# Kernel tuning notes

Measured on AMD Instinct MI355X. Metric: run time of the kernel, lower is better.

## Reference

```python
import jax, jax.numpy as jnp
import numpy as np

N = 50000      # nodes
E = 1600000    # edges (avg degree 32)
DIM = 128
HEADS = 8
HEAD_DIM = DIM // HEADS
HID = 4 * DIM          # hidden_multiplier=4 -> 512
FF_IN = 2 * DIM        # input_multiplier=2 (concat [h, message])
SCALE = 0.02


def setup_inputs() -> dict:
    key = jax.random.key(0)
    ks = jax.random.split(key, 13)
    h = jax.random.normal(ks[0], (N, DIM), dtype=jnp.float32)
    src = jax.random.randint(ks[1], (E,), 0, N, dtype=jnp.int32)
    dst = jax.random.randint(ks[2], (E,), 0, N, dtype=jnp.int32)
    W_in = jax.random.normal(ks[3], (DIM, DIM), dtype=jnp.float32) * SCALE
    b_in = jnp.zeros((DIM,), dtype=jnp.float32)
    Wu = jax.random.normal(ks[4], (DIM, HEADS), dtype=jnp.float32) * SCALE
    bu = jnp.zeros((HEADS,), dtype=jnp.float32)
    Wv = jax.random.normal(ks[5], (DIM, HEADS), dtype=jnp.float32) * SCALE  # no bias
    W1 = jax.random.normal(ks[6], (FF_IN, HID), dtype=jnp.float32) * SCALE
    b1 = jnp.zeros((HID,), dtype=jnp.float32)
    W2 = jax.random.normal(ks[7], (HID, DIM), dtype=jnp.float32) * SCALE
    b2 = jnp.zeros((DIM,), dtype=jnp.float32)
    return dict(h=h, W_in=W_in, b_in=b_in, Wu=Wu, bu=bu, Wv=Wv,
                W1=W1, b1=b1, W2=W2, b2=b2, src=src, dst=dst)


def reference(h, W_in, b_in, Wu, bu, Wv, W1, b1, W2, b2, src, dst):
    # input projection
    h1 = h @ W_in + b_in                                  # [N, DIM]
    attn_u = h1 @ Wu + bu                                 # [N, H]
    attn_v = h1 @ Wv                                      # [N, H]
    # u_add_v + LeakyReLU(0.2): per-edge scores
    scores = attn_u[src] + attn_v[dst]                    # [E, H]
    scores = jnp.where(scores >= 0, scores, 0.2 * scores)
    # edge_softmax: normalize over edges incoming to each dst node
    smax = jax.ops.segment_max(scores, dst, num_segments=N)  # [N, H]
    smax = jnp.where(jnp.isfinite(smax), smax, jnp.zeros_like(smax))
    e = jnp.exp(scores - smax[dst])                       # [E, H]
    denom = jax.ops.segment_sum(e, dst, num_segments=N)   # [N, H]
    probs = e / denom[dst]                                # [E, H]
    # u_mul_e_sum with h reshaped to [N, head_dim, heads]
    h_heads = h1.reshape(N, HEAD_DIM, HEADS)
    msg = jax.ops.segment_sum(h_heads[src] * probs[:, None, :], dst,
                              num_segments=N).reshape(N, DIM)
    # feed-forward on concat (dropout = identity in eval)
    combined = jnp.concatenate([h1, msg], axis=1)         # [N, 2*DIM]
    x = jax.nn.gelu(combined @ W1 + b1, approximate=False)
    return x @ W2 + b2                                    # [N, DIM]
```

## Files before the change

kernel.cpp:

```cpp
#include <hip/hip_runtime.h>
#include <hip/hip_fp16.h>
#include <math.h>

#define DIMM 128
#define NHEAD 8
#define SLOTS 96
#define QCAP32 4352
#define NSLICE 128
#define RS 6272
#define NPAD 50176

typedef __attribute__((ext_vector_type(8))) short bf16x8;
typedef __attribute__((ext_vector_type(4))) float f32x4;
typedef __attribute__((ext_vector_type(2))) float f32x2;
typedef __attribute__((ext_vector_type(4))) int i32x4;

#if defined(__has_builtin)
#if __has_builtin(__builtin_amdgcn_cvt_pk_f32_fp8)
#define HAS_CVT_FP8 1
#endif
#endif

__device__ __forceinline__ unsigned short f2bf(float x) {
    union { float f; unsigned int u; } v; v.f = x;
    unsigned int r = v.u + 0x7FFFu + ((v.u >> 16) & 1u);
    return (unsigned short)(r >> 16);
}
__device__ __forceinline__ float bf2f(unsigned short u) {
    union { unsigned int u; float f; } v; v.u = ((unsigned int)u) << 16;
    return v.f;
}
__device__ __forceinline__ unsigned char f2e4m3(float x) {
    union { float f; unsigned u; } v; v.f = x;
    unsigned s = (v.u >> 24) & 0x80u;
    unsigned au = v.u & 0x7fffffffu;
    unsigned r = au + 0xFFFFFu + ((au >> 20) & 1u);
    int E = (int)(r >> 23) - 120;
    if (E < 1) return (unsigned char)s;
    if (E > 15) E = 15;
    return (unsigned char)(s | (E << 3) | ((r >> 20) & 7u));
}
__device__ __forceinline__ float e4m32f(unsigned b) {
    unsigned em = b & 0x7fu;
    unsigned s = (b & 0x80u) << 24;
    unsigned u = s | ((em + 960u) << 20);
    union { unsigned u; float f; } v;
    v.u = em ? u : s;
    return v.f;
}
__device__ __forceinline__ float gelu_exact(float x) {
    return 0.5f * x * (1.0f + erff(x * 0.70710678118654752f));
}
__device__ __forceinline__ __half2 shfl_xor_h2(__half2 v, int d) {
    union { __half2 h; int i; } u; u.h = v;
    u.i = __shfl_xor(u.i, d, 64);
    return u.h;
}

__global__ __launch_bounds__(256) void k_prep0(
        const float* __restrict__ W_in,
        unsigned short* __restrict__ WiT_hi, unsigned short* __restrict__ WiT_lo)
{
    int i = blockIdx.x * 256 + threadIdx.x;
    if (i < 128 * 128) {
        int n = i >> 7, k = i & 127;
        float w = W_in[(size_t)k * 128 + n];
        unsigned short hi = f2bf(w);
        WiT_hi[i] = hi;
        WiT_lo[i] = f2bf(w - bf2f(hi));
    }
}

__global__ __launch_bounds__(256, 4) void k_front(
        const float* __restrict__ h,
        const unsigned short* __restrict__ WiT_hi,
        const unsigned short* __restrict__ WiT_lo,
        const float* __restrict__ b_in,
        const float* __restrict__ Wu, const float* __restrict__ bu,
        const float* __restrict__ Wv,
        const float* __restrict__ W1, const float* __restrict__ W2,
        const int* __restrict__ src, const int* __restrict__ dst,
        unsigned short* __restrict__ h1c,
        unsigned short* __restrict__ hg8,
        unsigned short* __restrict__ au, unsigned short* __restrict__ av,
        unsigned short* __restrict__ W1T, unsigned short* __restrict__ W2T,
        unsigned short* __restrict__ gh,
        unsigned int* __restrict__ gq,
        int* __restrict__ gqn,
        int N, int E, int NH1, int SC)
{
    __shared__ unsigned long long smem64[QCAP32 / 2];
    __shared__ unsigned int hist32[RS / 2];
    __shared__ int qn;
    int b = blockIdx.x;
    int t = threadIdx.x;

    if (b < SC) {
        unsigned int* q32 = (unsigned int*)smem64;
        int range = b & 7;
        int slice = b >> 3;
        for (int i = t; i < RS / 2; i += 256) hist32[i] = 0;
        if (t == 0) qn = 0;
        __syncthreads();
        int per = (((E + NSLICE - 1) / NSLICE) + 3) & ~3;
        int s0 = slice * per;
        int s1 = min(s0 + per, E);
        int base_d = range * RS;
        int lane = t & 63;
        for (int be = s0; be < s1; be += 1024) {
            int e0 = be + t * 4;
            int dv[4] = {-1, -1, -1, -1};
            if (e0 + 3 < s1) {
                i32x4 d4 = __builtin_nontemporal_load((const i32x4*)(dst + e0));
                dv[0] = d4.x; dv[1] = d4.y; dv[2] = d4.z; dv[3] = d4.w;
            } else if (e0 < s1) {
                dv[0] = dst[e0];
                if (e0 + 1 < s1) dv[1] = dst[e0 + 1];
                if (e0 + 2 < s1) dv[2] = dst[e0 + 2];
            }
            int dl[4];
            bool m[4];
            int mcnt = 0;
            #pragma unroll
            for (int k = 0; k < 4; ++k) {
                dl[k] = dv[k] - base_d;
                m[k] = (unsigned)dl[k] < (unsigned)RS;
                mcnt += m[k] ? 1 : 0;
            }
            int incl = mcnt;
            #pragma unroll
            for (int d = 1; d < 64; d <<= 1) {
                int v = __shfl_up(incl, d, 64);
                if (lane >= d) incl += v;
            }
            int wb = 0;
            if (lane == 63 && incl) wb = atomicAdd(&qn, incl);
            wb = __shfl(wb, 63, 64);
            int pos = wb + incl - mcnt;
            #pragma unroll
            for (int k = 0; k < 4; ++k) {
                if (m[k]) {
                    int s = __builtin_nontemporal_load(src + e0 + k);
                    atomicAdd(&hist32[dl[k] >> 1], 1u << ((dl[k] & 1) * 16));
                    if (pos < QCAP32)
                        q32[pos] = ((unsigned)dl[k] << 16) | ((unsigned)s & 0xffffu);
                    ++pos;
                }
            }
        }
        __syncthreads();
        int M = min(qn, QCAP32);
        for (int i = t; i < M; i += 256)
            gq[(size_t)b * QCAP32 + i] = q32[i];
        if (t == 0) gqn[b] = M;
        unsigned int* ghrow = (unsigned int*)(gh + (size_t)slice * NPAD + base_d);
        for (int i = t; i < RS / 2; i += 256) ghrow[i] = hist32[i];
        return;
    }
    if (b >= SC + NH1) {
        int i = (b - SC - NH1) * 256 + t;
        if (i < 256 * 512) {
            int k = i >> 9, j = i & 511;
            W1T[(size_t)j * 256 + k] = f2bf(W1[i]);
        }
        if (i < 512 * 128) {
            int k = i >> 7, j = i & 127;
            W2T[(size_t)j * 512 + k] = f2bf(W2[i]);
        }
        return;
    }

    unsigned short* Ahi = (unsigned short*)smem64;
    unsigned short* Alo = Ahi + 32 * 136;
    float* Wuv = (float*)hist32;
    int row0 = (b - SC) * 32;
    int lane = t & 63, wv = t >> 6;
    const int g = lane >> 4, r16 = lane & 15;

    for (int i = t; i < 2048; i += 256) {
        int k = i >> 4, hh = i & 15;
        Wuv[i] = (hh < 8) ? Wu[k * 8 + hh] : Wv[k * 8 + (hh - 8)];
    }

    #pragma unroll
    for (int u = 0; u < 4; ++u) {
        int idx = t + u * 256;
        int r = idx >> 5, c4 = idx & 31;
        float4 v = make_float4(0.f, 0.f, 0.f, 0.f);
        if (row0 + r < N) v = *(const float4*)(h + (size_t)(row0 + r) * DIMM + c4 * 4);
        unsigned short hi[4], lo[4];
        float vv[4] = {v.x, v.y, v.z, v.w};
        #pragma unroll
        for (int q = 0; q < 4; ++q) {
            hi[q] = f2bf(vv[q]);
            lo[q] = f2bf(vv[q] - bf2f(hi[q]));
        }
        unsigned int h01 = (unsigned)hi[0] | ((unsigned)hi[1] << 16);
        unsigned int h23 = (unsigned)hi[2] | ((unsigned)hi[3] << 16);
        unsigned int l01 = (unsigned)lo[0] | ((unsigned)lo[1] << 16);
        unsigned int l23 = (unsigned)lo[2] | ((unsigned)lo[3] << 16);
        *(uint2*)&Ahi[r * 136 + c4 * 4] = make_uint2(h01, h23);
        *(uint2*)&Alo[r * 136 + c4 * 4] = make_uint2(l01, l23);
    }
    __syncthreads();

    f32x4 acc[2][2];
    #pragma unroll
    for (int mf = 0; mf < 2; ++mf)
        #pragma unroll
        for (int nf = 0; nf < 2; ++nf)
            acc[mf][nf] = (f32x4){0.f, 0.f, 0.f, 0.f};

    for (int ks = 0; ks < 128; ks += 32) {
        bf16x8 ahi[2], alo[2], bhi[2], blo[2];
        #pragma unroll
        for (int mf = 0; mf < 2; ++mf) {
            ahi[mf] = *(const bf16x8*)&Ahi[(mf * 16 + r16) * 136 + ks + g * 8];
            alo[mf] = *(const bf16x8*)&Alo[(mf * 16 + r16) * 136 + ks + g * 8];
        }
        #pragma unroll
        for (int nf = 0; nf < 2; ++nf) {
            int coln = wv * 32 + nf * 16 + r16;
            bhi[nf] = *(const bf16x8*)(WiT_hi + (size_t)coln * 128 + ks + g * 8);
            blo[nf] = *(const bf16x8*)(WiT_lo + (size_t)coln * 128 + ks + g * 8);
        }
        #pragma unroll
        for (int mf = 0; mf < 2; ++mf)
            #pragma unroll
            for (int nf = 0; nf < 2; ++nf) {
                acc[mf][nf] = __builtin_amdgcn_mfma_f32_16x16x32_bf16(
                                  ahi[mf], bhi[nf], acc[mf][nf], 0, 0, 0);
                acc[mf][nf] = __builtin_amdgcn_mfma_f32_16x16x32_bf16(
                                  ahi[mf], blo[nf], acc[mf][nf], 0, 0, 0);
                acc[mf][nf] = __builtin_amdgcn_mfma_f32_16x16x32_bf16(
                                  alo[mf], bhi[nf], acc[mf][nf], 0, 0, 0);
            }
    }
    __syncthreads();

    #pragma unroll
    for (int nf = 0; nf < 2; ++nf) {
        int col = wv * 32 + nf * 16 + r16;
        float bb = b_in[col];
        #pragma unroll
        for (int mf = 0; mf < 2; ++mf) {
            #pragma unroll
            for (int q = 0; q < 4; ++q) {
                int row = mf * 16 + g * 4 + q;
                unsigned short hb = f2bf(acc[mf][nf][q] + bb);
                Ahi[row * 136 + col] = hb;
                if (row0 + row < N) h1c[(size_t)(row0 + row) * 128 + col] = hb;
            }
        }
    }
    __syncthreads();

    {
        int r = t >> 3;
        int j = t & 7;
        int hh2 = (j & 3) * 2;
        bool isv = (j >= 4);
        int hb = (isv ? 8 : 0) + hh2;
        float a0 = isv ? 0.f : bu[hh2];
        float a1 = isv ? 0.f : bu[hh2 + 1];
        for (int k = 0; k < 128; k += 8) {
            bf16x8 h8 = *(const bf16x8*)&Ahi[r * 136 + k];
            #pragma unroll
            for (int q = 0; q < 8; ++q) {
                float hv = bf2f((unsigned short)h8[q]);
                a0 = fmaf(hv, Wuv[(k + q) * 16 + hb], a0);
                a1 = fmaf(hv, Wuv[(k + q) * 16 + hb + 1], a1);
            }
        }
        if (row0 + r < N) {
            unsigned int pk = (unsigned)f2bf(a0) | ((unsigned)f2bf(a1) << 16);
            if (!isv) *(unsigned int*)(au + (size_t)(row0 + r) * 8 + hh2) = pk;
            else      *(unsigned int*)(av + (size_t)(row0 + r) * 8 + hh2) = pk;
        }
    }

    {
        int l = t & 63;
        int rg = t >> 6;
        #pragma unroll
        for (int rr = 0; rr < 8; ++rr) {
            int r2 = rg * 8 + rr;
            if (row0 + r2 < N) {
                unsigned lo8 = f2e4m3(bf2f(Ahi[r2 * 136 + l]));
                unsigned hi8 = f2e4m3(bf2f(Ahi[r2 * 136 + l + 64]));
                hg8[(size_t)(row0 + r2) * 64 + l] = (unsigned short)((hi8 << 8) | lo8);
            }
        }
    }
}

__global__ __launch_bounds__(256) void k_scan2(
        const unsigned short* __restrict__ gh,
        unsigned short* __restrict__ gb,
        int* __restrict__ cnt)
{
    int d = blockIdx.x * 256 + threadIdx.x;
    int sum = 0;
    #pragma unroll 8
    for (int s = 0; s < NSLICE; ++s) {
        gb[(size_t)s * NPAD + d] = (unsigned short)sum;
        sum += gh[(size_t)s * NPAD + d];
    }
    cnt[d] = sum;
}

__global__ __launch_bounds__(256) void k_place(
        const unsigned int* __restrict__ gq,
        const int* __restrict__ gqn,
        const unsigned short* __restrict__ gb,
        unsigned short* __restrict__ slots)
{
    __shared__ int bases[RS];
    int b = blockIdx.x;
    int range = b & 7, slice = b >> 3;
    int t = threadIdx.x;
    const unsigned short* gbrow = gb + (size_t)slice * NPAD + range * RS;
    for (int i = t; i < RS; i += 256) bases[i] = (int)gbrow[i];
    __syncthreads();
    int M = gqn[b];
    const unsigned int* q = gq + (size_t)b * QCAP32;
    for (int i = t; i < M; i += 256) {
        unsigned u = q[i];
        int dl = (int)(u >> 16);
        int slot = atomicAdd(&bases[dl], 1);
        if (slot < SLOTS)
            slots[(size_t)(range * RS + dl) * SLOTS + slot] = (unsigned short)(u & 0xffffu);
    }
}

__global__ __launch_bounds__(256) void k_agg(
        const unsigned short* __restrict__ hg8,
        const unsigned short* __restrict__ au,
        const unsigned short* __restrict__ av,
        const int* __restrict__ cnt, const unsigned short* __restrict__ slots,
        unsigned short* __restrict__ msgc,
        int N)
{
    __shared__ float p_lds[4][8][68];
    __shared__ int   s_lds[4][64];
    int t = threadIdx.x;
    int w = t >> 6, lane = t & 63;
    int n = blockIdx.x * 4 + w;
    if (n >= N) return;
    int deg = min(cnt[n], SLOTS);
    const unsigned short* myslots = slots + (size_t)n * SLOTS;
    unsigned short* msg_out = msgc + (size_t)n * 128;
    if (deg == 0) {
        msg_out[lane] = 0;
        msg_out[64 + lane] = 0;
        return;
    }

    float avf[8];
    {
        bf16x8 a8 = *(const bf16x8*)(av + (size_t)n * 8);
        #pragma unroll
        for (int hh = 0; hh < 8; ++hh) avf[hh] = bf2f((unsigned short)a8[hh]);
    }
    int hsel = lane & 7;
    float den = 0.f, accA = 0.f, accB = 0.f;

    for (int base = 0; base < deg; base += 64) {
        int nact = min(64, deg - base);
        bool act = (lane < nact);
        int sn = act ? (int)myslots[base + lane] : 0;
        float p[8];
        if (act) {
            bf16x8 u8 = *(const bf16x8*)(au + (size_t)sn * 8);
            #pragma unroll
            for (int hh = 0; hh < 8; ++hh) {
                float v = bf2f((unsigned short)u8[hh]) + avf[hh];
                v = (v >= 0.f) ? v : 0.2f * v;
                p[hh] = __expf(v);
            }
        } else {
            #pragma unroll
            for (int hh = 0; hh < 8; ++hh) p[hh] = 0.f;
        }

        __half2 PS[4];
        #pragma unroll
        for (int q = 0; q < 4; ++q) PS[q] = __floats2half2_rn(p[2*q], p[2*q+1]);
        #pragma unroll
        for (int d = 1; d < 8; d <<= 1) {
            #pragma unroll
            for (int q = 0; q < 4; ++q)
                PS[q] = __hadd2(PS[q], shfl_xor_h2(PS[q], d));
        }
        __half2 s01 = (hsel & 2) ? PS[1] : PS[0];
        __half2 s23 = (hsel & 2) ? PS[3] : PS[2];
        __half2 sel = (hsel & 4) ? s23 : s01;
        float csum_own = (hsel & 1) ? __high2float(sel) : __low2float(sel);
        #pragma unroll
        for (int d = 8; d < 64; d <<= 1)
            csum_own += __shfl_xor(csum_own, d, 64);
        den += csum_own;

        #pragma unroll
        for (int hh = 0; hh < 8; ++hh) p_lds[w][hh][lane] = p[hh];
        s_lds[w][lane] = sn;
        __threadfence_block();

        #pragma unroll 4
        for (int j = 0; j < nact; ++j) {
            int sj = s_lds[w][j];
            float pj = p_lds[w][hsel][j];
            unsigned int gg = (unsigned)hg8[(size_t)sj * 64 + lane];
#ifdef HAS_CVT_FP8
            f32x2 vv = __builtin_amdgcn_cvt_pk_f32_fp8((int)gg, false);
            accA = fmaf(pj, vv[0], accA);
            accB = fmaf(pj, vv[1], accB);
#else
            accA = fmaf(pj, e4m32f(gg & 0xffu), accA);
            accB = fmaf(pj, e4m32f(gg >> 8), accB);
#endif
        }
    }
    float inv = 1.0f / den;
    msg_out[lane] = f2bf(accA * inv);
    msg_out[64 + lane] = f2bf(accB * inv);
}

__global__ __launch_bounds__(256, 2) void k_ff(
        const unsigned short* __restrict__ h1c,
        const unsigned short* __restrict__ msgc,
        const unsigned short* __restrict__ W1T, const float* __restrict__ b1,
        const unsigned short* __restrict__ W2T, const float* __restrict__ b2,
        float* __restrict__ out, int N)
{
    __shared__ unsigned short smem[64 * 520];
    int t = threadIdx.x;
    int lane = t & 63, w = t >> 6;
    int row0 = blockIdx.x * 64;
    const int g = lane >> 4, r16 = lane & 15;

    #pragma unroll
    for (int u = 0; u < 8; ++u) {
        int idx = t + u * 256;
        int r = idx >> 5, c8 = idx & 31;
        bf16x8 v = {0, 0, 0, 0, 0, 0, 0, 0};
        if (row0 + r < N) {
            const unsigned short* sp = (c8 < 16)
                ? (h1c  + (size_t)(row0 + r) * 128 + c8 * 8)
                : (msgc + (size_t)(row0 + r) * 128 + (c8 - 16) * 8);
            v = *(const bf16x8*)sp;
        }
        *(bf16x8*)&smem[r * 264 + c8 * 8] = v;
    }
    __syncthreads();

    f32x4 acc[4][8];
    #pragma unroll
    for (int mf = 0; mf < 4; ++mf)
        #pragma unroll
        for (int nf = 0; nf < 8; ++nf)
            acc[mf][nf] = (f32x4){0.f, 0.f, 0.f, 0.f};

    int wcol = w * 128;
    for (int ks = 0; ks < 256; ks += 32) {
        bf16x8 a[4], b[8];
        #pragma unroll
        for (int mf = 0; mf < 4; ++mf)
            a[mf] = *(const bf16x8*)&smem[(mf * 16 + r16) * 264 + ks + g * 8];
        #pragma unroll
        for (int nf = 0; nf < 8; ++nf)
            b[nf] = *(const bf16x8*)(W1T + (size_t)(wcol + nf * 16 + r16) * 256 + ks + g * 8);
        #pragma unroll
        for (int mf = 0; mf < 4; ++mf)
            #pragma unroll
            for (int nf = 0; nf < 8; ++nf)
                acc[mf][nf] = __builtin_amdgcn_mfma_f32_16x16x32_bf16(
                                  a[mf], b[nf], acc[mf][nf], 0, 0, 0);
    }
    __syncthreads();

    #pragma unroll
    for (int nf = 0; nf < 8; ++nf) {
        int col = wcol + nf * 16 + r16;
        float bb = b1[col];
        #pragma unroll
        for (int mf = 0; mf < 4; ++mf) {
            #pragma unroll
            for (int q = 0; q < 4; ++q) {
                int row = mf * 16 + g * 4 + q;
                smem[row * 520 + col] = f2bf(gelu_exact(acc[mf][nf][q] + bb));
            }
        }
    }
    __syncthreads();

    f32x4 acc2[4][2];
    #pragma unroll
    for (int mf = 0; mf < 4; ++mf)
        #pragma unroll
        for (int nf = 0; nf < 2; ++nf)
            acc2[mf][nf] = (f32x4){0.f, 0.f, 0.f, 0.f};

    int ocol = w * 32;
    for (int ks = 0; ks < 512; ks += 32) {
        bf16x8 a[4], b[2];
        #pragma unroll
        for (int mf = 0; mf < 4; ++mf)
            a[mf] = *(const bf16x8*)&smem[(mf * 16 + r16) * 520 + ks + g * 8];
        #pragma unroll
        for (int nf = 0; nf < 2; ++nf)
            b[nf] = *(const bf16x8*)(W2T + (size_t)(ocol + nf * 16 + r16) * 512 + ks + g * 8);
        #pragma unroll
        for (int mf = 0; mf < 4; ++mf)
            #pragma unroll
            for (int nf = 0; nf < 2; ++nf)
                acc2[mf][nf] = __builtin_amdgcn_mfma_f32_16x16x32_bf16(
                                   a[mf], b[nf], acc2[mf][nf], 0, 0, 0);
    }

    #pragma unroll
    for (int nf = 0; nf < 2; ++nf) {
        int col = ocol + nf * 16 + r16;
        float bb = b2[col];
        #pragma unroll
        for (int mf = 0; mf < 4; ++mf) {
            #pragma unroll
            for (int q = 0; q < 4; ++q) {
                int row = row0 + mf * 16 + g * 4 + q;
                if (row < N)
                    out[(size_t)row * 128 + col] = acc2[mf][nf][q] + bb;
            }
        }
    }
}

extern "C" void kernel_launch(void* const* d_in, const int* in_sizes, int n_in,
                              void* d_out, int out_size, void* d_ws, size_t ws_size,
                              hipStream_t stream)
{
    const float* h    = (const float*)d_in[0];
    const float* W_in = (const float*)d_in[1];
    const float* b_in = (const float*)d_in[2];
    const float* Wu   = (const float*)d_in[3];
    const float* bu   = (const float*)d_in[4];
    const float* Wv   = (const float*)d_in[5];
    const float* W1   = (const float*)d_in[6];
    const float* b1   = (const float*)d_in[7];
    const float* W2   = (const float*)d_in[8];
    const float* b2   = (const float*)d_in[9];
    const int*   src  = (const int*)d_in[10];
    const int*   dst  = (const int*)d_in[11];
    int N = in_sizes[0] / DIMM;
    int E = in_sizes[10];
    float* out = (float*)d_out;

    char* ws = (char*)d_ws;
    size_t off = 0;
    auto alloc = [&](size_t bytes) -> void* {
        void* p = ws + off;
        off = (off + bytes + 255) & ~(size_t)255;
        return p;
    };
    unsigned short* h1c  = (unsigned short*)alloc((size_t)N * 128 * 2);
    unsigned short* hg8  = (unsigned short*)alloc((size_t)N * 64 * 2);
    unsigned short* msgc = (unsigned short*)alloc((size_t)N * 128 * 2);
    unsigned short* au   = (unsigned short*)alloc((size_t)N * 8 * 2);
    unsigned short* av   = (unsigned short*)alloc((size_t)N * 8 * 2);
    int* cnt        = (int*)alloc((size_t)NPAD * 4);
    unsigned short* slots = (unsigned short*)alloc((size_t)NPAD * SLOTS * 2);
    unsigned short* W1T = (unsigned short*)alloc((size_t)512 * 256 * 2);
    unsigned short* W2T = (unsigned short*)alloc((size_t)128 * 512 * 2);
    unsigned short* WiT_hi = (unsigned short*)alloc((size_t)128 * 128 * 2);
    unsigned short* WiT_lo = (unsigned short*)alloc((size_t)128 * 128 * 2);
    unsigned short* ghh = (unsigned short*)alloc((size_t)NSLICE * NPAD * 2);
    unsigned short* gb  = (unsigned short*)alloc((size_t)NSLICE * NPAD * 2);
    unsigned int* gq = (unsigned int*)alloc((size_t)NSLICE * 8 * QCAP32 * 4);
    int* gqn        = (int*)alloc((size_t)NSLICE * 8 * 4);

    int SC = NSLICE * 8;
    int NH1 = (N + 31) / 32;
    int GRID = SC + NH1 + 512;

    k_prep0<<<64, 256, 0, stream>>>(W_in, WiT_hi, WiT_lo);
    k_front<<<GRID, 256, 0, stream>>>(
        h, WiT_hi, WiT_lo, b_in, Wu, bu, Wv, W1, W2, src, dst,
        h1c, hg8, au, av, W1T, W2T, ghh, gq, gqn,
        N, E, NH1, SC);
    k_scan2<<<NPAD / 256, 256, 0, stream>>>(ghh, gb, cnt);
    k_place<<<SC, 256, 0, stream>>>(gq, gqn, gb, slots);
    k_agg<<<(N + 3) / 4, 256, 0, stream>>>(hg8, au, av, cnt, slots, msgc, N);
    k_ff<<<(N + 63) / 64, 256, 0, stream>>>(h1c, msgc, W1T, b1, W2T, b2, out, N);
}
```

Before: 240.3 us.

## Bucket edges by destination range in one pass per slice instead of per-range blocks

Each edge-binning block now reads its slice of src/dst once and scatters every edge into one of eight LDS queues by destination range. Per-range histograms are then built serially from those queues. Before, eight blocks per slice each reread the full dst slice, so this removes most of the redundant dst traffic. In exchange, the slice count doubles, which doubles the per-slice histogram arrays written here and scanned later. It also adds contended LDS atomics on eight queue counters and lowers the occupancy hint for the front kernel.

```diff
diff --git a/kernel.cpp b/kernel.cpp
--- a/kernel.cpp
+++ b/kernel.cpp
@@ -5,8 +5,8 @@
 #define DIMM 128
 #define NHEAD 8
 #define SLOTS 96
-#define QCAP32 4352
-#define NSLICE 128
+#define QCAP 1024
+#define NSLICE 256
 #define RS 6272
 #define NPAD 50176
 
@@ -71,7 +71,7 @@
     }
 }
 
-__global__ __launch_bounds__(256, 4) void k_front(
+__global__ __launch_bounds__(256, 3) void k_front(
         const float* __restrict__ h,
         const unsigned short* __restrict__ WiT_hi,
         const unsigned short* __restrict__ WiT_lo,
@@ -89,72 +89,64 @@
         int* __restrict__ gqn,
         int N, int E, int NH1, int SC)
 {
-    __shared__ unsigned long long smem64[QCAP32 / 2];
-    __shared__ unsigned int hist32[RS / 2];
-    __shared__ int qn;
+    __shared__ unsigned int smemU[8 * QCAP + RS / 2];
+    __shared__ int qn[8];
     int b = blockIdx.x;
     int t = threadIdx.x;
 
     if (b < SC) {
-        unsigned int* q32 = (unsigned int*)smem64;
-        int range = b & 7;
-        int slice = b >> 3;
-        for (int i = t; i < RS / 2; i += 256) hist32[i] = 0;
-        if (t == 0) qn = 0;
+        unsigned int* q8 = smemU;
+        unsigned int* hist32 = smemU + 8 * QCAP;
+        int ss = b;
+        if (t < 8) qn[t] = 0;
         __syncthreads();
-        int per = (((E + NSLICE - 1) / NSLICE) + 3) & ~3;
-        int s0 = slice * per;
+        int per = (((E + SC - 1) / SC) + 3) & ~3;
+        int s0 = ss * per;
         int s1 = min(s0 + per, E);
-        int base_d = range * RS;
-        int lane = t & 63;
         for (int be = s0; be < s1; be += 1024) {
             int e0 = be + t * 4;
-            int dv[4] = {-1, -1, -1, -1};
+            int dv[4], sv[4];
+            int nv = 0;
             if (e0 + 3 < s1) {
                 i32x4 d4 = __builtin_nontemporal_load((const i32x4*)(dst + e0));
+                i32x4 s4 = __builtin_nontemporal_load((const i32x4*)(src + e0));
                 dv[0] = d4.x; dv[1] = d4.y; dv[2] = d4.z; dv[3] = d4.w;
+                sv[0] = s4.x; sv[1] = s4.y; sv[2] = s4.z; sv[3] = s4.w;
+                nv = 4;
             } else if (e0 < s1) {
-                dv[0] = dst[e0];
-                if (e0 + 1 < s1) dv[1] = dst[e0 + 1];
-                if (e0 + 2 < s1) dv[2] = dst[e0 + 2];
-            }
-            int dl[4];
-            bool m[4];
-            int mcnt = 0;
+                nv = s1 - e0;
+                for (int k = 0; k < nv; ++k) { dv[k] = dst[e0 + k]; sv[k] = src[e0 + k]; }
+            }
             #pragma unroll
             for (int k = 0; k < 4; ++k) {
-                dl[k] = dv[k] - base_d;
-                m[k] = (unsigned)dl[k] < (unsigned)RS;
-                mcnt += m[k] ? 1 : 0;
-            }
-            int incl = mcnt;
-            #pragma unroll
-            for (int d = 1; d < 64; d <<= 1) {
-                int v = __shfl_up(incl, d, 64);
-                if (lane >= d) incl += v;
-            }
-            int wb = 0;
-            if (lane == 63 && incl) wb = atomicAdd(&qn, incl);
-            wb = __shfl(wb, 63, 64);
-            int pos = wb + incl - mcnt;
-            #pragma unroll
-            for (int k = 0; k < 4; ++k) {
-                if (m[k]) {
-                    int s = __builtin_nontemporal_load(src + e0 + k);
-                    atomicAdd(&hist32[dl[k] >> 1], 1u << ((dl[k] & 1) * 16));
-                    if (pos < QCAP32)
-                        q32[pos] = ((unsigned)dl[k] << 16) | ((unsigned)s & 0xffffu);
-                    ++pos;
+                if (k < nv) {
+                    int d = dv[k];
+                    int rng = d / RS;
+                    int dl = d - rng * RS;
+                    int pos = atomicAdd(&qn[rng], 1);
+                    if (pos < QCAP)
+                        q8[rng * QCAP + pos] = ((unsigned)dl << 16) | ((unsigned)sv[k] & 0xffffu);
                 }
             }
         }
         __syncthreads();
-        int M = min(qn, QCAP32);
-        for (int i = t; i < M; i += 256)
-            gq[(size_t)b * QCAP32 + i] = q32[i];
-        if (t == 0) gqn[b] = M;
-        unsigned int* ghrow = (unsigned int*)(gh + (size_t)slice * NPAD + base_d);
-        for (int i = t; i < RS / 2; i += 256) ghrow[i] = hist32[i];
+        for (int r = 0; r < 8; ++r) {
+            for (int i = t; i < RS / 2; i += 256) hist32[i] = 0;
+            __syncthreads();
+            int M = min(qn[r], QCAP);
+            unsigned int* dq = gq + (size_t)(ss * 8 + r) * QCAP;
+            for (int i = t; i < M; i += 256) {
+                unsigned u = q8[r * QCAP + i];
+                unsigned dl = u >> 16;
+                atomicAdd(&hist32[dl >> 1], 1u << ((dl & 1) * 16));
+                dq[i] = u;
+            }
+            __syncthreads();
+            unsigned int* ghrow = (unsigned int*)(gh + (size_t)ss * NPAD + r * RS);
+            for (int i = t; i < RS / 2; i += 256) ghrow[i] = hist32[i];
+            if (t == 0) gqn[ss * 8 + r] = M;
+            __syncthreads();
+        }
         return;
     }
     if (b >= SC + NH1) {
@@ -170,9 +162,9 @@
         return;
     }
 
-    unsigned short* Ahi = (unsigned short*)smem64;
+    unsigned short* Ahi = (unsigned short*)smemU;
     unsigned short* Alo = Ahi + 32 * 136;
-    float* Wuv = (float*)hist32;
+    float* Wuv = (float*)(smemU + 4352);
     int row0 = (b - SC) * 32;
     int lane = t & 63, wv = t >> 6;
     const int g = lane >> 4, r16 = lane & 15;
@@ -323,7 +315,7 @@
     for (int i = t; i < RS; i += 256) bases[i] = (int)gbrow[i];
     __syncthreads();
     int M = gqn[b];
-    const unsigned int* q = gq + (size_t)b * QCAP32;
+    const unsigned int* q = gq + (size_t)b * QCAP;
     for (int i = t; i < M; i += 256) {
         unsigned u = q[i];
         int dl = (int)(u >> 16);
@@ -574,10 +566,10 @@
     unsigned short* WiT_lo = (unsigned short*)alloc((size_t)128 * 128 * 2);
     unsigned short* ghh = (unsigned short*)alloc((size_t)NSLICE * NPAD * 2);
     unsigned short* gb  = (unsigned short*)alloc((size_t)NSLICE * NPAD * 2);
-    unsigned int* gq = (unsigned int*)alloc((size_t)NSLICE * 8 * QCAP32 * 4);
+    unsigned int* gq = (unsigned int*)alloc((size_t)NSLICE * 8 * QCAP * 4);
     int* gqn        = (int*)alloc((size_t)NSLICE * 8 * 4);
 
-    int SC = NSLICE * 8;
+    int SC = NSLICE;
     int NH1 = (N + 31) / 32;
     int GRID = SC + NH1 + 512;
 
@@ -587,7 +579,7 @@
         h1c, hg8, au, av, W1T, W2T, ghh, gq, gqn,
         N, E, NH1, SC);
     k_scan2<<<NPAD / 256, 256, 0, stream>>>(ghh, gb, cnt);
-    k_place<<<SC, 256, 0, stream>>>(gq, gqn, gb, slots);
+    k_place<<<NSLICE * 8, 256, 0, stream>>>(gq, gqn, gb, slots);
     k_agg<<<(N + 3) / 4, 256, 0, stream>>>(hg8, au, av, cnt, slots, msgc, N);
     k_ff<<<(N + 63) / 64, 256, 0, stream>>>(h1c, msgc, W1T, b1, W2T, b2, out, N);
 }
```

Result: faster. 220.2 us (median of 2 runs) (-8.3%).
